# Kernel tuning notes

Measured on AMD Instinct MI355X. Metric: run time of the kernel, lower is better.

Reference implementation:

```python
import jax, jax.numpy as jnp
import numpy as np
import math

B, T, C = 4, 2048, 1024
H = 16
DH = C // H
SCALE = 1.0 / math.sqrt(DH)


def setup_inputs() -> dict:
    key = jax.random.key(0)
    k1, k2, k3 = jax.random.split(key, 3)
    x = jax.random.normal(k1, (B, T, C), dtype=jnp.float32)
    # init_unit_norm: randn / sqrt(d_in)
    W_qkv = jax.random.normal(k2, (3 * C, C), dtype=jnp.float32) / math.sqrt(C)
    W_out = jax.random.normal(k3, (C, C), dtype=jnp.float32) / math.sqrt(C)
    return {"x": x, "W_qkv": W_qkv, "W_out": W_out}


def reference(x, W_qkv, W_out):
    b, t, c = x.shape
    qkv = x @ W_qkv.T                      # [B,T,3C]
    q, k, v = jnp.split(qkv, 3, axis=-1)
    # [B,T,C] -> [B,H,T,Dh]
    q = q.reshape(b, t, H, DH).transpose(0, 2, 1, 3)
    k = k.reshape(b, t, H, DH).transpose(0, 2, 1, 3)
    v = v.reshape(b, t, H, DH).transpose(0, 2, 1, 3)
    scores = jnp.einsum('bhtd,bhsd->bhts', q, k) * SCALE  # [B,H,T,T]
    mask = jnp.tril(jnp.ones((t, t), dtype=bool))
    scores = jnp.where(mask, scores, 0.0)  # no softmax
    attn = jnp.einsum('bhts,bhsd->bhtd', scores, v)       # [B,H,T,Dh]
    attn = attn.transpose(0, 2, 1, 3).reshape(b, t, c)
    return attn @ W_out.T
```

## Files before the change

kernel.cpp:

```cpp
#include <hip/hip_runtime.h>

#define TT 2048
#define CC 1024

typedef __attribute__((ext_vector_type(8))) __bf16 bf16x8;
typedef __attribute__((ext_vector_type(4))) float f32x4;
typedef unsigned int u32;
typedef __attribute__((ext_vector_type(2))) u32 u32x2;

__device__ __forceinline__ short f2bf(float f) {
  u32 u = __float_as_uint(f);
  u += 0x7fffu + ((u >> 16) & 1u);
  return (short)(u >> 16);
}

#if __has_builtin(__builtin_amdgcn_cvt_pk_bf16_f32)
__device__ __forceinline__ u32 pack2(float a, float b) {
  auto v = __builtin_amdgcn_cvt_pk_bf16_f32(a, b);
  return __builtin_bit_cast(u32, v);
}
#else
__device__ __forceinline__ u32 pack2(float a, float b) {
  u32 ua = __float_as_uint(a), ub = __float_as_uint(b);
  ua += 0x7fffu + ((ua >> 16) & 1u);
  ub += 0x7fffu + ((ub >> 16) & 1u);
  return (ua >> 16) | (ub & 0xffff0000u);
}
#endif

__global__ __launch_bounds__(256) void cvt_all(const float* __restrict__ x,
                                               const float* __restrict__ wqkv,
                                               const float* __restrict__ wout,
                                               short* __restrict__ dst) {
  int i = blockIdx.x * blockDim.x + threadIdx.x;
  const float* src;
  float sc = 1.0f;
  if (i < 2097152) {
    src = x + (size_t)i * 4;
  } else if (i < 2883584) {
    int j = i - 2097152;
    src = wqkv + (size_t)j * 4;
    if (j < 262144) sc = 0.125f;
  } else {
    src = wout + (size_t)(i - 2883584) * 4;
  }
  float4 f = *reinterpret_cast<const float4*>(src);
  short4 s;
  s.x = f2bf(f.x * sc); s.y = f2bf(f.y * sc); s.z = f2bf(f.z * sc); s.w = f2bf(f.w * sc);
  reinterpret_cast<short4*>(dst)[i] = s;
}

__device__ __forceinline__ void storev(float* p, float v) { *p = v; }
__device__ __forceinline__ void storev(short* p, float v) { *p = f2bf(v); }

#if __has_builtin(__builtin_amdgcn_global_load_lds)
#define HAVE_GLD_LDS 1
__device__ __forceinline__ void gld_lds16(const short* g, short* l) {
  __builtin_amdgcn_global_load_lds((const __attribute__((address_space(1))) u32*)g,
                                   (__attribute__((address_space(3))) u32*)l, 16, 0, 0);
}
#endif

__device__ __forceinline__ f32x4 mfma16(bf16x8 a, bf16x8 b, f32x4 c) {
  return __builtin_amdgcn_mfma_f32_16x16x32_bf16(a, b, c, 0, 0, 0);
}

template <int NN>
__device__ __forceinline__ void waitvm() {
  if constexpr (NN == 0) asm volatile("s_waitcnt vmcnt(0)" ::: "memory");
  else if constexpr (NN == 3) asm volatile("s_waitcnt vmcnt(3)" ::: "memory");
  else if constexpr (NN == 4) asm volatile("s_waitcnt vmcnt(4)" ::: "memory");
  else if constexpr (NN == 6) asm volatile("s_waitcnt vmcnt(6)" ::: "memory");
  else if constexpr (NN == 8) asm volatile("s_waitcnt vmcnt(8)" ::: "memory");
}

#define GNOOP ((void)0)
#define GPHASE4(DB, KS, STG, SYNC)                         \
  {                                                        \
    bf16x8 af[MFRAG], bfr[NFR];                            \
    ldA(af, DB, KS);                                       \
    ldB(bfr, DB, KS);                                      \
    STG;                                                   \
    __builtin_amdgcn_s_setprio(1);                         \
    mmaAll(af, bfr);                                       \
    __builtin_amdgcn_s_setprio(0);                         \
    asm volatile("s_waitcnt lgkmcnt(0)" ::: "memory");     \
    SYNC;                                                  \
    __builtin_amdgcn_s_barrier();                          \
  }

template <typename OutT, int N, int K, int BM, int BN>
__global__ __launch_bounds__(512, 2) void gemm4p(const short* __restrict__ A,
                                                 const short* __restrict__ B,
                                                 OutT* __restrict__ Cm) {
  constexpr int MFRAG = BM / 32;
  constexpr int NFR = BN / 64;
  constexpr int AGLD = BM / 128;
  constexpr int BGLD = BN / 128;
  constexpr int GPP = AGLD + BGLD;
  constexpr int SYNCN = 2 * GPP;
  constexpr int NT = K / 64, NITER = NT / 2;
  constexpr int DBS = 64 * (BM + BN);
  constexpr int TMX = (8192 / BM) / 8;
  extern __shared__ short lds[];
  const int tid = threadIdx.x;
  const int wave = tid >> 6, lane = tid & 63;
  const int quad = lane >> 4, nl = lane & 15;
  const int wm = wave >> 2, wn = wave & 3;

  const int id = blockIdx.x;
  const int xcd = id & 7, slot = id >> 3;
  const int mt = xcd * TMX + (slot % TMX);
  const int nt = slot / TMX;
  const int m0 = mt * BM, n0 = nt * BN;

  const int srow = lane >> 2;
  const int sperm = ((lane & 3) ^ ((lane >> 3) & 3)) * 8;
  const short* pA = A + (size_t)(m0 + wave * (BM / 8) + srow) * K + sperm;
  const short* pB = B + (size_t)(n0 + wave * (BN / 8) + srow) * K + sperm;

  const int perm = (quad ^ ((nl >> 1) & 3)) * 8;

  f32x4 acc[MFRAG][NFR] = {};

  auto stageA = [&](int db, int ks, int t) {
    const short* s = pA + (size_t)t * 64 + ks * 32;
    short* d = lds + db * DBS + ks * (BM * 32) + wave * (BM * 4);
#pragma unroll
    for (int j = 0; j < AGLD; ++j) {
#if HAVE_GLD_LDS
      gld_lds16(s + (size_t)j * 16 * K, d + j * 512);
#else
      *reinterpret_cast<uint4*>(d + j * 512 + lane * 8) =
          *reinterpret_cast<const uint4*>(s + (size_t)j * 16 * K);
#endif
    }
  };
  auto stageB = [&](int db, int ks, int t) {
    const short* s = pB + (size_t)t * 64 + ks * 32;
    short* d = lds + db * DBS + BM * 64 + ks * (BN * 32) + wave * (BN * 4);
#pragma unroll
    for (int j = 0; j < BGLD; ++j) {
#if HAVE_GLD_LDS
      gld_lds16(s + (size_t)j * 16 * K, d + j * 512);
#else
      *reinterpret_cast<uint4*>(d + j * 512 + lane * 8) =
          *reinterpret_cast<const uint4*>(s + (size_t)j * 16 * K);
#endif
    }
  };
  auto stage = [&](int db, int ks, int t) { stageA(db, ks, t); stageB(db, ks, t); };

  auto ldA = [&](bf16x8 (&af)[MFRAG], int db, int ks) {
#pragma unroll
    for (int mf = 0; mf < MFRAG; ++mf)
      af[mf] = *reinterpret_cast<const bf16x8*>(
          &lds[db * DBS + ks * (BM * 32) + (wm * (BM / 2) + mf * 16 + nl) * 32 + perm]);
  };
  auto ldB = [&](bf16x8 (&bfr)[NFR], int db, int ks) {
#pragma unroll
    for (int nf = 0; nf < NFR; ++nf)
      bfr[nf] = *reinterpret_cast<const bf16x8*>(
          &lds[db * DBS + BM * 64 + ks * (BN * 32) + (wn * (BN / 4) + nf * 16 + nl) * 32 + perm]);
  };
  auto mmaAll = [&](const bf16x8 (&af)[MFRAG], const bf16x8 (&bfr)[NFR]) {
#pragma unroll
    for (int mf = 0; mf < MFRAG; ++mf)
#pragma unroll
      for (int nf = 0; nf < NFR; ++nf)
        acc[mf][nf] = mfma16(af[mf], bfr[nf], acc[mf][nf]);
  };

  stage(0, 0, 0); stage(0, 1, 0); stage(1, 0, 1);
  waitvm<SYNCN>();
  __builtin_amdgcn_s_barrier();

  for (int i = 0; i < NITER - 1; ++i) {
    GPHASE4(0, 0, stage(1, 1, 2 * i + 1), waitvm<SYNCN>())
    GPHASE4(0, 1, stage(0, 0, 2 * i + 2), waitvm<SYNCN>())
    GPHASE4(1, 0, stage(0, 1, 2 * i + 2), waitvm<SYNCN>())
    GPHASE4(1, 1, stage(1, 0, 2 * i + 3), waitvm<SYNCN>())
  }
  GPHASE4(0, 0, stage(1, 1, NT - 1), waitvm<SYNCN>())
  GPHASE4(0, 1, GNOOP, waitvm<GPP>())
  GPHASE4(1, 0, GNOOP, waitvm<0>())
  GPHASE4(1, 1, GNOOP, GNOOP)

#pragma unroll
  for (int mf = 0; mf < MFRAG; ++mf) {
    const int row = m0 + wm * (BM / 2) + mf * 16 + quad * 4;
#pragma unroll
    for (int nf = 0; nf < NFR; ++nf) {
      const int col = n0 + wn * (BN / 4) + nf * 16 + nl;
#pragma unroll
      for (int r = 0; r < 4; ++r)
        storev(&Cm[(size_t)(row + r) * N + col], acc[mf][nf][r]);
    }
  }
}

__global__ __launch_bounds__(256) void transpose_v(const short* __restrict__ qkv,
                                                   short* __restrict__ vt) {
  __shared__ short Ls[64 * 68];
  const int bh = blockIdx.y, tb = blockIdx.x;
  const int b = bh >> 4, h = bh & 15;
  const int tid = threadIdx.x;
  const short* src = qkv + (size_t)(b * TT + tb * 64) * (3 * CC) + 2 * CC + h * 64;
#pragma unroll
  for (int i = 0; i < 2; ++i) {
    int idx = tid + i * 256;
    int tl = idx >> 3, dc = idx & 7;
    uint4 d4 = *reinterpret_cast<const uint4*>(&src[(size_t)tl * (3 * CC) + dc * 8]);
    *reinterpret_cast<uint2*>(&Ls[tl * 68 + dc * 8]) = make_uint2(d4.x, d4.y);
    *reinterpret_cast<uint2*>(&Ls[tl * 68 + dc * 8 + 4]) = make_uint2(d4.z, d4.w);
  }
  __syncthreads();
  short* dst = vt + (size_t)(bh * 64) * TT + tb * 64;
#pragma unroll
  for (int i = 0; i < 2; ++i) {
    int idx = tid + i * 256;
    int dl = idx >> 3, tc = idx & 7;
    short tmp[8];
#pragma unroll
    for (int j = 0; j < 8; ++j) tmp[j] = Ls[(tc * 8 + j) * 68 + dl];
    *reinterpret_cast<uint4*>(&dst[(size_t)dl * TT + tc * 8]) = *reinterpret_cast<uint4*>(tmp);
  }
}

template <bool DIAG>
__device__ __forceinline__ void attn_compute(const short* kf, const short* vf, u32* ssw,
                                             const bf16x8 (&qf)[2][2], f32x4 (&o)[2][4],
                                             int lane, int quad, int nl) {
  bf16x8 k00 = *reinterpret_cast<const bf16x8*>(&kf[0 * 512 + lane * 8]);
  bf16x8 k01 = *reinterpret_cast<const bf16x8*>(&kf[1 * 512 + lane * 8]);
  bf16x8 k10 = *reinterpret_cast<const bf16x8*>(&kf[2 * 512 + lane * 8]);
  bf16x8 k11 = *reinterpret_cast<const bf16x8*>(&kf[3 * 512 + lane * 8]);
  bf16x8 vB[4];
#pragma unroll
  for (int nb = 0; nb < 4; ++nb)
    vB[nb] = *reinterpret_cast<const bf16x8*>(&vf[nb * 512 + lane * 8]);
  const int sig = (nl >> 1) & 3;
  const int plo = (((quad >> 1) ^ sig) << 2) | ((quad * 2) & 3);
  const int phi = (((2 + (quad >> 1)) ^ sig) << 2) | ((quad * 2) & 3);
  const int prd = ((quad ^ sig) << 2);
  {
    u32* srow = &ssw[0 * 256 + nl * 16];
    f32x4 s0 = {};
    s0 = mfma16(k00, qf[0][0], s0);
    s0 = mfma16(k01, qf[0][1], s0);
    if (DIAG) {
#pragma unroll
      for (int r = 0; r < 4; ++r) s0[r] = (quad * 4 + r <= nl) ? s0[r] : 0.0f;
    }
    *reinterpret_cast<u32x2*>(&srow[plo]) = u32x2{pack2(s0[0], s0[1]), pack2(s0[2], s0[3])};
    if (DIAG) {
      *reinterpret_cast<u32x2*>(&srow[phi]) = u32x2{0u, 0u};
    } else {
      f32x4 s1 = {};
      s1 = mfma16(k10, qf[0][0], s1);
      s1 = mfma16(k11, qf[0][1], s1);
      *reinterpret_cast<u32x2*>(&srow[phi]) = u32x2{pack2(s1[0], s1[1]), pack2(s1[2], s1[3])};
    }
  }
  {
    u32* srow = &ssw[1 * 256 + nl * 16];
    f32x4 s0 = {}, s1 = {};
    s0 = mfma16(k00, qf[1][0], s0);
    s0 = mfma16(k01, qf[1][1], s0);
    s1 = mfma16(k10, qf[1][0], s1);
    s1 = mfma16(k11, qf[1][1], s1);
    if (DIAG) {
#pragma unroll
      for (int r = 0; r < 4; ++r) s1[r] = (quad * 4 + r <= nl) ? s1[r] : 0.0f;
    }
    *reinterpret_cast<u32x2*>(&srow[plo]) = u32x2{pack2(s0[0], s0[1]), pack2(s0[2], s0[3])};
    *reinterpret_cast<u32x2*>(&srow[phi]) = u32x2{pack2(s1[0], s1[1]), pack2(s1[2], s1[3])};
  }
#pragma unroll
  for (int m = 0; m < 2; ++m) {
    bf16x8 sf = *reinterpret_cast<const bf16x8*>(&ssw[m * 256 + nl * 16 + prd]);
#pragma unroll
    for (int nb = 0; nb < 4; ++nb) o[m][nb] = mfma16(sf, vB[nb], o[m][nb]);
  }
}

__global__ __launch_bounds__(256, 4) void attn_kernel(const short* __restrict__ qkv,
                                                      const short* __restrict__ vt,
                                                      short* __restrict__ attnb) {
  const int gid = blockIdx.x;
  const int xcd = gid & 7, slot = gid >> 3;
  const int bh = xcd * 8 + (slot & 7);
  const int ti = 15 - (slot >> 3);
  const int b = bh >> 4, h = bh & 15;
  const int T0 = ti * 128;
  const int tid = threadIdx.x;
  const int wave = tid >> 6, lane = tid & 63;
  const int quad = lane >> 4, nl = lane & 15;

  const short* qbase = qkv + (size_t)(b * TT) * (3 * CC) + h * 64;
  const short* kbase = qbase + CC;
  const short* vbase = vt + (size_t)(bh * 64) * TT;

  __shared__ __align__(16) short Frag[2][8192];
  __shared__ __align__(16) u32 Ss[4][512];
  u32* ssw = Ss[wave];

  const int tw0 = T0 + wave * 32;
  bf16x8 qf[2][2];
#pragma unroll
  for (int m = 0; m < 2; ++m)
#pragma unroll
    for (int half = 0; half < 2; ++half)
      qf[m][half] = *reinterpret_cast<const bf16x8*>(
          &qbase[(size_t)(tw0 + m * 16 + nl) * (3 * CC) + half * 32 + quad * 8]);

  f32x4 o[2][4] = {};

  const short* ksrc = kbase + (size_t)(wave * 16 + nl) * (3 * CC) + quad * 8;
  const int sp_w = wave >> 1, nb0 = (wave & 1) * 2;
  const short* vsrc0 = vbase + (size_t)((nb0 + 0) * 16 + nl) * TT + sp_w * 32 + quad * 8;
  const short* vsrc1 = vbase + (size_t)((nb0 + 1) * 16 + nl) * TT + sp_w * 32 + quad * 8;

  auto stage = [&](short* fb, int c) {
    const size_t koff = (size_t)(c * 64) * (3 * CC);
#if HAVE_GLD_LDS
    gld_lds16(ksrc + koff, &fb[(2 * wave) * 512]);
    gld_lds16(ksrc + koff + 32, &fb[(2 * wave + 1) * 512]);
    gld_lds16(vsrc0 + c * 64, &fb[4096 + (2 * wave) * 512]);
    gld_lds16(vsrc1 + c * 64, &fb[4096 + (2 * wave + 1) * 512]);
#else
    *reinterpret_cast<uint4*>(&fb[(2 * wave) * 512 + lane * 8]) =
        *reinterpret_cast<const uint4*>(ksrc + koff);
    *reinterpret_cast<uint4*>(&fb[(2 * wave + 1) * 512 + lane * 8]) =
        *reinterpret_cast<const uint4*>(ksrc + koff + 32);
    *reinterpret_cast<uint4*>(&fb[4096 + (2 * wave) * 512 + lane * 8]) =
        *reinterpret_cast<const uint4*>(vsrc0 + c * 64);
    *reinterpret_cast<uint4*>(&fb[4096 + (2 * wave + 1) * 512 + lane * 8]) =
        *reinterpret_cast<const uint4*>(vsrc1 + c * 64);
#endif
  };

  const int nch = 2 * ti + 2;
  const int cd = 4 * ti + wave;

  stage(Frag[0], 0);
  for (int c = 0; c < nch; ++c) {
    __syncthreads();
    if (c + 1 < nch) stage(Frag[(c + 1) & 1], c + 1);
    const short* fb = Frag[c & 1];
    const int c0 = 2 * c, c1 = 2 * c + 1;
    if (c0 < cd)
      attn_compute<false>(fb, fb + 4096, ssw, qf, o, lane, quad, nl);
    else if (c0 == cd)
      attn_compute<true>(fb, fb + 4096, ssw, qf, o, lane, quad, nl);
    if (c1 < cd)
      attn_compute<false>(fb + 2048, fb + 4096 + 2048, ssw, qf, o, lane, quad, nl);
    else if (c1 == cd)
      attn_compute<true>(fb + 2048, fb + 4096 + 2048, ssw, qf, o, lane, quad, nl);
  }

#pragma unroll
  for (int m = 0; m < 2; ++m)
#pragma unroll
    for (int nb = 0; nb < 4; ++nb)
#pragma unroll
      for (int r = 0; r < 4; ++r) {
        int t = tw0 + m * 16 + quad * 4 + r;
        attnb[(size_t)(b * TT + t) * CC + h * 64 + nb * 16 + nl] = f2bf(o[m][nb][r]);
      }
}

extern "C" void kernel_launch(void* const* d_in, const int* in_sizes, int n_in,
                              void* d_out, int out_size, void* d_ws, size_t ws_size,
                              hipStream_t stream) {
  const float* x = (const float*)d_in[0];
  const float* wqkv = (const float*)d_in[1];
  const float* wout = (const float*)d_in[2];
  float* out = (float*)d_out;

  char* ws = (char*)d_ws;
  short* xb    = (short*)(ws);
  short* wqkvb = (short*)(ws + 16777216);
  short* woutb = (short*)(ws + 23068672);
  short* qkvb  = (short*)(ws + 25165824);
  short* attnb = (short*)(ws + 75497472);
  short* vt    = xb;

  static bool inited = false;
  if (!inited) {
    (void)hipFuncSetAttribute(reinterpret_cast<const void*>(&gemm4p<short, 3072, 1024, 128, 384>),
                              hipFuncAttributeMaxDynamicSharedMemorySize, 131072);
    (void)hipFuncSetAttribute(reinterpret_cast<const void*>(&gemm4p<float, 1024, 1024, 128, 256>),
                              hipFuncAttributeMaxDynamicSharedMemorySize, 98304);
    inited = true;
  }

  cvt_all<<<12288, 256, 0, stream>>>(x, wqkv, wout, xb);

  gemm4p<short, 3072, 1024, 128, 384><<<512, 512, 131072, stream>>>(xb, wqkvb, qkvb);

  transpose_v<<<dim3(32, 64), 256, 0, stream>>>(qkvb, vt);

  attn_kernel<<<1024, 256, 0, stream>>>(qkvb, vt, attnb);

  gemm4p<float, 1024, 1024, 128, 256><<<256, 512, 98304, stream>>>(attnb, woutb, out);
}
```

Before: 229.6 us.

## Fuse V transpose into QKV GEMM epilogue, drop separate transpose kernel

The QKV projection GEMM now writes Q and K into a compact [B*T, 2C] buffer and writes V directly in transposed [B*H*Dh, T] layout from its epilogue. This removes the transpose_v kernel launch and the round trip of V through global memory. Attention reads Q and K with the narrower 2C row stride. The transposed V stores are 8-byte writes of four consecutive t values, so they are less coalesced than the row-major stores and may cost more in the GEMM epilogue.

```diff
diff --git a/kernel.cpp b/kernel.cpp
--- a/kernel.cpp
+++ b/kernel.cpp
@@ -89,10 +89,11 @@
     __builtin_amdgcn_s_barrier();                          \
   }
 
-template <typename OutT, int N, int K, int BM, int BN>
+template <typename OutT, int N, int K, int BM, int BN, bool SPLITV>
 __global__ __launch_bounds__(512, 2) void gemm4p(const short* __restrict__ A,
                                                  const short* __restrict__ B,
-                                                 OutT* __restrict__ Cm) {
+                                                 OutT* __restrict__ Cm,
+                                                 short* __restrict__ Vt) {
   constexpr int MFRAG = BM / 32;
   constexpr int NFR = BN / 64;
   constexpr int AGLD = BM / 128;
@@ -102,6 +103,7 @@
   constexpr int NT = K / 64, NITER = NT / 2;
   constexpr int DBS = 64 * (BM + BN);
   constexpr int TMX = (8192 / BM) / 8;
+  constexpr int CSTRIDE = SPLITV ? 2048 : N;
   extern __shared__ short lds[];
   const int tid = threadIdx.x;
   const int wave = tid >> 6, lane = tid & 63;
@@ -192,38 +194,21 @@
 #pragma unroll
     for (int nf = 0; nf < NFR; ++nf) {
       const int col = n0 + wn * (BN / 4) + nf * 16 + nl;
-#pragma unroll
-      for (int r = 0; r < 4; ++r)
-        storev(&Cm[(size_t)(row + r) * N + col], acc[mf][nf][r]);
-    }
-  }
-}
-
-__global__ __launch_bounds__(256) void transpose_v(const short* __restrict__ qkv,
-                                                   short* __restrict__ vt) {
-  __shared__ short Ls[64 * 68];
-  const int bh = blockIdx.y, tb = blockIdx.x;
-  const int b = bh >> 4, h = bh & 15;
-  const int tid = threadIdx.x;
-  const short* src = qkv + (size_t)(b * TT + tb * 64) * (3 * CC) + 2 * CC + h * 64;
-#pragma unroll
-  for (int i = 0; i < 2; ++i) {
-    int idx = tid + i * 256;
-    int tl = idx >> 3, dc = idx & 7;
-    uint4 d4 = *reinterpret_cast<const uint4*>(&src[(size_t)tl * (3 * CC) + dc * 8]);
-    *reinterpret_cast<uint2*>(&Ls[tl * 68 + dc * 8]) = make_uint2(d4.x, d4.y);
-    *reinterpret_cast<uint2*>(&Ls[tl * 68 + dc * 8 + 4]) = make_uint2(d4.z, d4.w);
-  }
-  __syncthreads();
-  short* dst = vt + (size_t)(bh * 64) * TT + tb * 64;
-#pragma unroll
-  for (int i = 0; i < 2; ++i) {
-    int idx = tid + i * 256;
-    int dl = idx >> 3, tc = idx & 7;
-    short tmp[8];
-#pragma unroll
-    for (int j = 0; j < 8; ++j) tmp[j] = Ls[(tc * 8 + j) * 68 + dl];
-    *reinterpret_cast<uint4*>(&dst[(size_t)dl * TT + tc * 8]) = *reinterpret_cast<uint4*>(tmp);
+      bool isv = false;
+      if constexpr (SPLITV) isv = (col >= 2048);
+      if (isv) {
+        const int feat = col - 2048;
+        const int b = row >> 11, t = row & 2047;
+        short4 v4;
+        v4.x = f2bf(acc[mf][nf][0]); v4.y = f2bf(acc[mf][nf][1]);
+        v4.z = f2bf(acc[mf][nf][2]); v4.w = f2bf(acc[mf][nf][3]);
+        *reinterpret_cast<short4*>(&Vt[((size_t)(b << 10) + feat) * 2048 + t]) = v4;
+      } else {
+#pragma unroll
+        for (int r = 0; r < 4; ++r)
+          storev(&Cm[(size_t)(row + r) * CSTRIDE + col], acc[mf][nf][r]);
+      }
+    }
   }
 }
 
@@ -284,7 +269,7 @@
   }
 }
 
-__global__ __launch_bounds__(256, 4) void attn_kernel(const short* __restrict__ qkv,
+__global__ __launch_bounds__(256, 4) void attn_kernel(const short* __restrict__ qk,
                                                       const short* __restrict__ vt,
                                                       short* __restrict__ attnb) {
   const int gid = blockIdx.x;
@@ -297,7 +282,7 @@
   const int wave = tid >> 6, lane = tid & 63;
   const int quad = lane >> 4, nl = lane & 15;
 
-  const short* qbase = qkv + (size_t)(b * TT) * (3 * CC) + h * 64;
+  const short* qbase = qk + (size_t)(b * TT) * (2 * CC) + h * 64;
   const short* kbase = qbase + CC;
   const short* vbase = vt + (size_t)(bh * 64) * TT;
 
@@ -312,17 +297,17 @@
 #pragma unroll
     for (int half = 0; half < 2; ++half)
       qf[m][half] = *reinterpret_cast<const bf16x8*>(
-          &qbase[(size_t)(tw0 + m * 16 + nl) * (3 * CC) + half * 32 + quad * 8]);
+          &qbase[(size_t)(tw0 + m * 16 + nl) * (2 * CC) + half * 32 + quad * 8]);
 
   f32x4 o[2][4] = {};
 
-  const short* ksrc = kbase + (size_t)(wave * 16 + nl) * (3 * CC) + quad * 8;
+  const short* ksrc = kbase + (size_t)(wave * 16 + nl) * (2 * CC) + quad * 8;
   const int sp_w = wave >> 1, nb0 = (wave & 1) * 2;
   const short* vsrc0 = vbase + (size_t)((nb0 + 0) * 16 + nl) * TT + sp_w * 32 + quad * 8;
   const short* vsrc1 = vbase + (size_t)((nb0 + 1) * 16 + nl) * TT + sp_w * 32 + quad * 8;
 
   auto stage = [&](short* fb, int c) {
-    const size_t koff = (size_t)(c * 64) * (3 * CC);
+    const size_t koff = (size_t)(c * 64) * (2 * CC);
 #if HAVE_GLD_LDS
     gld_lds16(ksrc + koff, &fb[(2 * wave) * 512]);
     gld_lds16(ksrc + koff + 32, &fb[(2 * wave + 1) * 512]);
@@ -382,26 +367,27 @@
   short* xb    = (short*)(ws);
   short* wqkvb = (short*)(ws + 16777216);
   short* woutb = (short*)(ws + 23068672);
-  short* qkvb  = (short*)(ws + 25165824);
+  short* qk    = (short*)(ws + 25165824);
+  short* vt    = (short*)(ws + 58720256);
   short* attnb = (short*)(ws + 75497472);
-  short* vt    = xb;
 
   static bool inited = false;
   if (!inited) {
-    (void)hipFuncSetAttribute(reinterpret_cast<const void*>(&gemm4p<short, 3072, 1024, 128, 384>),
-                              hipFuncAttributeMaxDynamicSharedMemorySize, 131072);
-    (void)hipFuncSetAttribute(reinterpret_cast<const void*>(&gemm4p<float, 1024, 1024, 128, 256>),
-                              hipFuncAttributeMaxDynamicSharedMemorySize, 98304);
+    (void)hipFuncSetAttribute(
+        reinterpret_cast<const void*>(&gemm4p<short, 3072, 1024, 128, 384, true>),
+        hipFuncAttributeMaxDynamicSharedMemorySize, 131072);
+    (void)hipFuncSetAttribute(
+        reinterpret_cast<const void*>(&gemm4p<float, 1024, 1024, 128, 256, false>),
+        hipFuncAttributeMaxDynamicSharedMemorySize, 98304);
     inited = true;
   }
 
   cvt_all<<<12288, 256, 0, stream>>>(x, wqkv, wout, xb);
 
-  gemm4p<short, 3072, 1024, 128, 384><<<512, 512, 131072, stream>>>(xb, wqkvb, qkvb);
-
-  transpose_v<<<dim3(32, 64), 256, 0, stream>>>(qkvb, vt);
-
-  attn_kernel<<<1024, 256, 0, stream>>>(qkvb, vt, attnb);
-
-  gemm4p<float, 1024, 1024, 128, 256><<<256, 512, 98304, stream>>>(attnb, woutb, out);
-}
+  gemm4p<short, 3072, 1024, 128, 384, true><<<512, 512, 131072, stream>>>(xb, wqkvb, qk, vt);
+
+  attn_kernel<<<1024, 256, 0, stream>>>(qk, vt, attnb);
+
+  gemm4p<float, 1024, 1024, 128, 256, false><<<256, 512, 98304, stream>>>(attnb, woutb, out,
+                                                                          nullptr);
+}
```

Measured after the change: 226.9 us. No clear change (-1.2%).
